# Kernel tuning notes

Measured on AMD Instinct MI355X. Metric: run time of the kernel, lower is better.

The kernel has to match this reference:

```python
import jax, jax.numpy as jnp
import numpy as np
import math

B, S, D_IN, D, H, L, NC = 4, 2048, 64, 512, 8, 2, 2
DK = D // H
FACTOR = 5
TOPK = min(FACTOR * int(math.log(S)), S)  # 35
EPS = 1e-5


def make_pe():
    # sinusoidal positional encoding [S, D]
    pos = jnp.arange(S, dtype=jnp.float32)[:, None]
    div = jnp.exp(jnp.arange(0, D, 2, dtype=jnp.float32) * (-math.log(10000.0) / D))
    pe = jnp.zeros((S, D), jnp.float32)
    pe = pe.at[:, 0::2].set(jnp.sin(pos * div)).at[:, 1::2].set(jnp.cos(pos * div))
    return pe


def layernorm(x, g, b):
    m = x.mean(-1, keepdims=True)
    v = x.var(-1, keepdims=True)
    return (x - m) / jnp.sqrt(v + EPS) * g + b


def setup_inputs() -> dict:
    key = jax.random.key(0)
    ks = iter(jax.random.split(key, 16))
    def p(shape, s=0.02):
        return jax.random.normal(next(ks), shape, jnp.float32) * s
    return dict(
        x=jax.random.normal(next(ks), (B, S, D_IN), jnp.float32),
        emb_w=p((D_IN, D)), emb_b=jnp.zeros((D,), jnp.float32),
        wq=p((L, D, D)), bq=jnp.zeros((L, D), jnp.float32),
        wk=p((L, D, D)), bk=jnp.zeros((L, D), jnp.float32),
        wv=p((L, D, D)), bv=jnp.zeros((L, D), jnp.float32),
        wo=p((L, D, D)), bo=jnp.zeros((L, D), jnp.float32),
        ff1_w=p((L, D, 4 * D)), ff1_b=jnp.zeros((L, 4 * D), jnp.float32),
        ff2_w=p((L, 4 * D, D)), ff2_b=jnp.zeros((L, D), jnp.float32),
        ln1_g=jnp.ones((L, D), jnp.float32), ln1_b=jnp.zeros((L, D), jnp.float32),
        ln2_g=jnp.ones((L, D), jnp.float32), ln2_b=jnp.zeros((L, D), jnp.float32),
        dec1_w=p((D, D // 2)), dec1_b=jnp.zeros((D // 2,), jnp.float32),
        dec2_w=p((D // 2, NC)), dec2_b=jnp.zeros((NC,), jnp.float32),
    )


def reference(x, emb_w, emb_b, wq, bq, wk, bk, wv, bv, wo, bo,
              ff1_w, ff1_b, ff2_w, ff2_b, ln1_g, ln1_b, ln2_g, ln2_b,
              dec1_w, dec1_b, dec2_w, dec2_b):
    h = x @ emb_w + emb_b + make_pe()[None]  # [B,S,D]
    scale = 1.0 / math.sqrt(DK)
    for i in range(L):
        q = (h @ wq[i] + bq[i]).reshape(B, S, H, DK).transpose(0, 2, 1, 3)
        k = (h @ wk[i] + bk[i]).reshape(B, S, H, DK).transpose(0, 2, 1, 3)
        v = (h @ wv[i] + bv[i]).reshape(B, S, H, DK).transpose(0, 2, 1, 3)
        scores = jnp.einsum('bhqd,bhkd->bhqk', q, k) * scale  # [B,H,S,S]
        top_scores, _ = jax.lax.top_k(scores, TOPK)            # [B,H,S,TOPK]
        attn = jax.nn.softmax(top_scores, axis=-1)
        # NOTE: faithful to source quirk — V sliced to its FIRST TOPK rows,
        # top_indices are discarded by the original module.
        ao = jnp.einsum('bhqk,bhkd->bhqd', attn, v[:, :, :TOPK, :])
        ao = ao.transpose(0, 2, 1, 3).reshape(B, S, D) @ wo[i] + bo[i]
        h = layernorm(h + ao, ln1_g[i], ln1_b[i])
        ff = jax.nn.relu(h @ ff1_w[i] + ff1_b[i]) @ ff2_w[i] + ff2_b[i]
        h = layernorm(h + ff, ln2_g[i], ln2_b[i])
    pooled = h.mean(axis=1)  # AdaptiveAvgPool1d(1) over seq
    out = jax.nn.relu(pooled @ dec1_w + dec1_b) @ dec2_w + dec2_b  # [B,NC]
    return out
```

## Files before the change

kernel.cpp:

```cpp
#include <hip/hip_runtime.h>
#include <cmath>

typedef unsigned short u16;
typedef __attribute__((ext_vector_type(8))) short short8;
typedef __attribute__((ext_vector_type(4))) float float4v;
typedef unsigned short ushort2v __attribute__((ext_vector_type(2)));

#define S_LEN 2048
#define NTOK  8192
#define TOPK  35
#define NT512 ((size_t)NTOK*512)

__device__ __forceinline__ u16 f2b(float f){
  unsigned int x = __float_as_uint(f);
  unsigned int r = (x + 0x7fffu + ((x >> 16) & 1u)) >> 16;
  return (u16)r;
}
__device__ __forceinline__ float b2f(u16 u){
  return __uint_as_float(((unsigned int)u) << 16);
}

__device__ __forceinline__ unsigned key_of(float f){
  unsigned u = (unsigned)f2b(f);
  unsigned m = (u & 0x8000u) ? 0xFFFFu : 0x8000u;
  return (u ^ m) & 0xFFFFu;
}
__device__ __forceinline__ float key_to_f(unsigned key){
  unsigned m = (key & 0x8000u) ? 0x8000u : 0xFFFFu;
  return __uint_as_float(((key ^ m) & 0xFFFFu) << 16);
}
__device__ __forceinline__ unsigned pkmax(unsigned a, unsigned b){
  union { unsigned u; ushort2v v; } x, y, r;
  x.u = a; y.u = b;
  r.v = __builtin_elementwise_max(x.v, y.v);
  return r.u;
}
__device__ __forceinline__ unsigned pkmin(unsigned a, unsigned b){
  union { unsigned u; ushort2v v; } x, y, r;
  x.u = a; y.u = b;
  r.v = __builtin_elementwise_min(x.v, y.v);
  return r.u;
}

__device__ __forceinline__ void bsort128(unsigned &v0, unsigned &v1, int l){
  #pragma unroll
  for (int k = 2; k <= 128; k <<= 1){
    #pragma unroll
    for (int j = k >> 1; j > 0; j >>= 1){
      if (j == 64){
        unsigned hi = pkmax(v0, v1), lo = pkmin(v0, v1);
        v0 = hi; v1 = lo;
      } else {
        unsigned o0 = (unsigned)__shfl_xor((int)v0, j, 64);
        unsigned o1 = (unsigned)__shfl_xor((int)v1, j, 64);
        bool up0 = (((l & k) == 0) != ((l & j) != 0));
        bool up1 = ((((64 + l) & k) == 0) != ((l & j) != 0));
        unsigned hi0 = pkmax(v0, o0), lo0 = pkmin(v0, o0);
        unsigned hi1 = pkmax(v1, o1), lo1 = pkmin(v1, o1);
        v0 = up0 ? hi0 : lo0;
        v1 = up1 ? hi1 : lo1;
      }
    }
  }
}

__device__ __forceinline__ void gload16(const void* g, void* l){
  __builtin_amdgcn_global_load_lds(
      (const __attribute__((address_space(1))) unsigned int*)g,
      (__attribute__((address_space(3))) unsigned int*)l, 16, 0, 0);
}

struct WtArgs {
  const float* wq; const float* wk; const float* wv; const float* wo;
  const float* ff1w; const float* ff2w;
  u16* wt_qkv; u16* wt_wo; u16* wt_ff1; u16* wt_ff2;
};
__global__ void prep_kernel(WtArgs a,
                            const float* __restrict__ x, const float* __restrict__ w,
                            const float* __restrict__ bias, float* __restrict__ h,
                            u16* __restrict__ h16){
  __shared__ float xs[4][64];
  __shared__ u16 t[32][33];
  int bx = blockIdx.x;
  int tid = threadIdx.x;
  if (bx < 6144){
    int l  = (bx >= 3072) ? 1 : 0;
    int tt = bx - l*3072;
    const float* W; u16* Wt; int K, N, tx_, ty_;
    if (tt < 1024){
      int seg = tt >> 8, r = tt & 255;
      tx_ = r & 15; ty_ = r >> 4; K = 512; N = 512;
      if (seg == 0){ W = a.wq + (size_t)l*262144; Wt = a.wt_qkv + (size_t)l*786432; }
      else if (seg == 1){ W = a.wk + (size_t)l*262144; Wt = a.wt_qkv + (size_t)l*786432 + 262144; }
      else if (seg == 2){ W = a.wv + (size_t)l*262144; Wt = a.wt_qkv + (size_t)l*786432 + 524288; }
      else { W = a.wo + (size_t)l*262144; Wt = a.wt_wo + (size_t)l*262144; }
    } else if (tt < 2048){
      int r = tt - 1024;
      tx_ = r & 63; ty_ = r >> 6; K = 512; N = 2048;
      W = a.ff1w + (size_t)l*1048576; Wt = a.wt_ff1 + (size_t)l*1048576;
    } else {
      int r = tt - 2048;
      tx_ = r & 15; ty_ = r >> 4; K = 2048; N = 512;
      W = a.ff2w + (size_t)l*1048576; Wt = a.wt_ff2 + (size_t)l*1048576;
    }
    int k0 = ty_*32, n0 = tx_*32;
    int tx = tid & 31, ty = tid >> 5;
    #pragma unroll
    for (int i = ty; i < 32; i += 8)
      t[i][tx] = f2b(W[(size_t)(k0+i)*N + n0+tx]);
    __syncthreads();
    #pragma unroll
    for (int i = ty; i < 32; i += 8)
      Wt[(size_t)(n0+i)*K + k0+tx] = t[tx][i];
  } else {
    int t0 = (bx - 6144) * 4;
    xs[tid >> 6][tid & 63] = x[(size_t)(t0 + (tid >> 6))*64 + (tid & 63)];
    __syncthreads();
    float b0 = bias[tid], b1 = bias[tid + 256];
    float acc[4][2];
    #pragma unroll
    for (int tk = 0; tk < 4; ++tk){ acc[tk][0] = b0; acc[tk][1] = b1; }
    #pragma unroll 8
    for (int k = 0; k < 64; ++k){
      float w0 = w[k*512 + tid];
      float w1 = w[k*512 + tid + 256];
      #pragma unroll
      for (int tk = 0; tk < 4; ++tk){
        float xv = xs[tk][k];
        acc[tk][0] += xv * w0;
        acc[tk][1] += xv * w1;
      }
    }
    const float neg_ln1e4_over_D = -9.210340371976184f / 512.f;
    int c0 = tid, c1 = tid + 256;
    float e0 = expf((float)(c0 & ~1) * neg_ln1e4_over_D);
    float e1 = expf((float)(c1 & ~1) * neg_ln1e4_over_D);
    #pragma unroll
    for (int tk = 0; tk < 4; ++tk){
      int tok = t0 + tk;
      int s = tok & (S_LEN - 1);
      float a0 = (float)s * e0;
      float p0 = (c0 & 1) ? cosf(a0) : sinf(a0);
      float a1 = (float)s * e1;
      float p1 = (c1 & 1) ? cosf(a1) : sinf(a1);
      float v0 = acc[tk][0] + p0, v1 = acc[tk][1] + p1;
      h[(size_t)tok*512 + c0] = v0;  h16[(size_t)tok*512 + c0] = f2b(v0);
      h[(size_t)tok*512 + c1] = v1;  h16[(size_t)tok*512 + c1] = f2b(v1);
    }
  }
}

template<int EPI>
__global__ __launch_bounds__(256) void gemm_mfma(
    const u16* __restrict__ A, int lda, const u16* __restrict__ Bt, int ldb,
    const float* __restrict__ bias0, const float* __restrict__ bias1,
    const float* __restrict__ bias2,
    float* __restrict__ Cf, u16* __restrict__ C16a, u16* __restrict__ C16b,
    float* __restrict__ Cv, int M, int N, int Klen){
  __shared__ __align__(16) u16 As[128*64];
  __shared__ __align__(16) u16 Bs[128*64];
  int tid = threadIdx.x;
  int w = tid >> 6, l = tid & 63, quad = l >> 4, m = l & 15;
  int gx = gridDim.x;
  int orig = blockIdx.y * gx + blockIdx.x;
  int nwg  = gx * gridDim.y;
  int tt   = (orig & 7) * (nwg >> 3) + (orig >> 3);
  int m0 = (tt / gx) * 128, n0 = (tt % gx) * 128;
  int mh = (w >> 1)*64, nh = (w & 1)*64;
  float4v acc[4][4];
  #pragma unroll
  for (int i = 0; i < 4; ++i)
    #pragma unroll
    for (int j = 0; j < 4; ++j) acc[i][j] = (float4v){0.f,0.f,0.f,0.f};

  for (int kt = 0; kt < Klen; kt += 64){
    #pragma unroll
    for (int c = 0; c < 4; ++c){
      int g = c*256 + tid;
      int row = g >> 3, sc = g & 7, dc = sc ^ (row & 7);
      gload16(A  + (size_t)(m0+row)*lda + kt + dc*8, As + (size_t)g*8);
      gload16(Bt + (size_t)(n0+row)*ldb + kt + dc*8, Bs + (size_t)g*8);
    }
    __syncthreads();
    #pragma unroll
    for (int kk = 0; kk < 2; ++kk){
      short8 af[4], bf[4];
      #pragma unroll
      for (int i = 0; i < 4; ++i){
        int dcx = kk*4 + quad;
        int ra = mh + i*16 + m;
        af[i] = *(const short8*)(As + (size_t)(ra*8 + (dcx ^ (ra & 7)))*8);
        int rb = nh + i*16 + m;
        bf[i] = *(const short8*)(Bs + (size_t)(rb*8 + (dcx ^ (rb & 7)))*8);
      }
      #pragma unroll
      for (int i = 0; i < 4; ++i)
        #pragma unroll
        for (int j = 0; j < 4; ++j)
          acc[i][j] = __builtin_amdgcn_mfma_f32_16x16x32_bf16(af[i], bf[j], acc[i][j], 0, 0, 0);
    }
    __syncthreads();
  }

  #pragma unroll
  for (int i = 0; i < 4; ++i){
    #pragma unroll
    for (int j = 0; j < 4; ++j){
      int col = n0 + nh + j*16 + m;
      #pragma unroll
      for (int r = 0; r < 4; ++r){
        int row = m0 + mh + i*16 + quad*4 + r;
        float v = acc[i][j][r];
        if (EPI == 0){
          Cf[(size_t)row*N + col] = v + bias0[col];
        } else if (EPI == 1){
          C16a[(size_t)row*N + col] = f2b(fmaxf(v + bias0[col], 0.f));
        } else {
          int sel = col >> 9, n5 = col & 511;
          const float* bp = (sel == 0) ? bias0 : (sel == 1) ? bias1 : bias2;
          float vv = v + bp[n5];
          int d = n5 & 63, hh = n5 >> 6;
          int b = row >> 11, s = row & 2047;
          size_t idx = (((size_t)(b*8 + hh))*2048 + s)*64 + d;
          if (sel == 0)      C16a[idx] = f2b(vv);
          else if (sel == 1) C16b[idx] = f2b(vv);
          else               Cv[idx]  = vv;
        }
      }
    }
  }
}

__global__ __launch_bounds__(512, 8) void attn_mfma_topk(
    const u16* __restrict__ qb16, const u16* __restrict__ kb16,
    const float* __restrict__ vb, u16* __restrict__ aob16){
  __shared__ unsigned pr[8*1024];
  int tid  = threadIdx.x;
  int w    = tid >> 6, l = tid & 63;
  int quad = l >> 4,  m = l & 15;
  int orig = blockIdx.y * 128 + blockIdx.x;
  int t4   = ((orig & 7) << 9) | (orig >> 3);
  int bh   = t4 >> 7;
  int q0   = (t4 & 127) << 4;

  const u16* Qp = qb16 + ((size_t)bh*2048 + q0 + m)*64 + quad*8;
  short8 a0 = *(const short8*)Qp;
  short8 a1 = *(const short8*)(Qp + 32);

  const u16* Kbase = kb16 + (size_t)bh*2048*64;
  unsigned sc[32];
  int swz = (quad & 1) << 4;
  const u16* kp0 = Kbase + (size_t)(w*128 + m)*64 + quad*8;
  const uint4* p4 = (const uint4*)(pr + w*1024);

  short8 cb0 = *(const short8*)kp0;
  short8 cb1 = *(const short8*)(kp0 + 32);
  #pragma unroll
  for (int t = 0; t < 16; ++t){
    short8 nb0, nb1;
    if (t < 15){
      int tn = t + 1;
      const u16* np = kp0 + (size_t)(((tn >> 3) << 10) + ((tn & 7) << 4))*64;
      nb0 = *(const short8*)np;
      nb1 = *(const short8*)(np + 32);
    }
    float4v acc = {0.f, 0.f, 0.f, 0.f};
    acc = __builtin_amdgcn_mfma_f32_16x16x32_bf16(a0, cb0, acc, 0, 0, 0);
    acc = __builtin_amdgcn_mfma_f32_16x16x32_bf16(a1, cb1, acc, 0, 0, 0);
    int lk = (w << 7) + ((t & 7) << 4);
    #pragma unroll
    for (int c = 0; c < 2; ++c){
      unsigned lo = key_of(acc[2*c]);
      unsigned hi = key_of(acc[2*c+1]);
      pr[(quad*2 + c)*1024 + ((lk + m) ^ swz)] = lo | (hi << 16);
    }
    cb0 = nb0; cb1 = nb1;
    if (t == 7){
      __syncthreads();
      #pragma unroll
      for (int j = 0; j < 4; ++j){
        uint4 v4 = p4[j*64 + l];
        sc[j*4+0] = v4.x; sc[j*4+1] = v4.y; sc[j*4+2] = v4.z; sc[j*4+3] = v4.w;
      }
      __syncthreads();
    }
  }
  __syncthreads();
  #pragma unroll
  for (int j = 0; j < 4; ++j){
    uint4 v4 = p4[j*64 + l];
    sc[16+j*4+0] = v4.x; sc[16+j*4+1] = v4.y; sc[16+j*4+2] = v4.z; sc[16+j*4+3] = v4.w;
  }

  unsigned* row = &pr[w*1024];

  unsigned m1 = pkmax(sc[0], sc[1]);
  unsigned m2 = pkmin(sc[0], sc[1]);
  #pragma unroll
  for (int i = 2; i < 32; ++i){
    unsigned v = sc[i];
    unsigned nm1 = pkmax(m1, v);
    m2 = pkmax(m2, pkmin(m1, v));
    m1 = nm1;
  }

  unsigned mA1 = m1 & 0xFFFFu, mB1 = m1 >> 16;
  unsigned mA2 = m2 & 0xFFFFu, mB2 = m2 >> 16;
  unsigned tA = 0, tB = 0;
  #pragma unroll
  for (int bit = 15; bit >= 0; --bit){
    unsigned cA = tA | (1u << bit);
    unsigned cB = tB | (1u << bit);
    int nA = __popcll(__ballot(mA1 >= cA)) + __popcll(__ballot(mA2 >= cA));
    int nB = __popcll(__ballot(mB1 >= cB)) + __popcll(__ballot(mB2 >= cB));
    if (nA >= TOPK) tA = cA;
    if (nB >= TOPK) tB = cB;
  }
  unsigned TT = (tA - 1) | ((tB - 1) << 16);

  unsigned mask = 0;
  #pragma unroll
  for (int i = 0; i < 32; ++i){
    mask |= (pkmax(sc[i], TT) != TT) ? (1u << i) : 0u;
  }
  int cnt = __popc(mask);

  int pre = cnt;
  #pragma unroll
  for (int off = 1; off < 64; off <<= 1){
    int n = __shfl_up(pre, off, 64);
    if (l >= off) pre += n;
  }
  pre -= cnt;

  #pragma unroll
  for (int i = 0; i < 32; ++i){
    if (mask & (1u << i)){
      int p = pre + __popc(mask & ((1u << i) - 1u));
      if (p < 128) row[p] = sc[i];
    }
  }
  int tot = __shfl(pre + cnt, 63, 64);

  unsigned c0 = (l < tot)      ? row[l]      : 0u;
  unsigned c1 = (64 + l < tot) ? row[64 + l] : 0u;

  const float* Vb = vb + (size_t)bh*2048*64 + l;
  float vreg[TOPK];
  #pragma unroll
  for (int r = 0; r < TOPK; ++r) vreg[r] = Vb[(size_t)r*64];

  bsort128(c0, c1, l);

  unsigned top0 = (unsigned)__shfl((int)c0, 0, 64);
  float mAf = key_to_f(top0 & 0xFFFFu) * 0.125f;
  float mBf = key_to_f(top0 >> 16)     * 0.125f;
  float tvA = key_to_f(c0 & 0xFFFFu)   * 0.125f;
  float tvB = key_to_f(c0 >> 16)       * 0.125f;
  float wAv = (l < TOPK) ? __expf(tvA - mAf) : 0.f;
  float wBv = (l < TOPK) ? __expf(tvB - mBf) : 0.f;

  float dA = wAv, dB = wBv;
  #pragma unroll
  for (int off = 32; off > 0; off >>= 1){
    dA += __shfl_xor(dA, off, 64);
    dB += __shfl_xor(dB, off, 64);
  }

  float accA = 0.f, accB = 0.f;
  #pragma unroll
  for (int r = 0; r < TOPK; ++r){
    float wA = __uint_as_float((unsigned)__builtin_amdgcn_readlane((int)__float_as_uint(wAv), r));
    float wB = __uint_as_float((unsigned)__builtin_amdgcn_readlane((int)__float_as_uint(wBv), r));
    float vv = vreg[r];
    accA += wA * vv;
    accB += wB * vv;
  }
  accA *= __builtin_amdgcn_rcpf(dA);
  accB *= __builtin_amdgcn_rcpf(dB);

  int b = bh >> 3, hh = bh & 7;
  int sA = q0 + w*2;
  aob16[(((size_t)(b*2048 + sA))*8 + hh)*64 + l]     = f2b(accA);
  aob16[(((size_t)(b*2048 + sA + 1))*8 + hh)*64 + l] = f2b(accB);
}

__global__ void resid_ln_kernel(float* __restrict__ h, const float* __restrict__ t,
                                const float* __restrict__ g, const float* __restrict__ b,
                                u16* __restrict__ h16){
  int half = threadIdx.x >> 7;
  int tok  = blockIdx.x*2 + half;
  int tid  = threadIdx.x & 127;
  size_t base4 = (size_t)tok * 128;
  float4 hv = ((const float4*)h)[base4 + tid];
  float4 tv = ((const float4*)t)[base4 + tid];
  float x0 = hv.x + tv.x, x1 = hv.y + tv.y;
  float x2 = hv.z + tv.z, x3 = hv.w + tv.w;
  __shared__ float red[8];
  int wid = threadIdx.x >> 6, lane = threadIdx.x & 63;

  float s = (x0 + x1) + (x2 + x3);
  #pragma unroll
  for (int off = 32; off > 0; off >>= 1) s += __shfl_xor(s, off, 64);
  if (lane == 0) red[wid] = s;
  __syncthreads();
  int hb = half << 1;
  float mean = (red[hb] + red[hb+1]) * (1.f/512.f);

  float d0 = x0 - mean, d1 = x1 - mean, d2 = x2 - mean, d3 = x3 - mean;
  float sq = (d0*d0 + d1*d1) + (d2*d2 + d3*d3);
  #pragma unroll
  for (int off = 32; off > 0; off >>= 1) sq += __shfl_xor(sq, off, 64);
  if (lane == 0) red[4 + wid] = sq;
  __syncthreads();
  float var = (red[4 + hb] + red[4 + hb + 1]) * (1.f/512.f);
  float inv = rsqrtf(var + 1e-5f);
  float4 gv = ((const float4*)g)[tid];
  float4 bv = ((const float4*)b)[tid];
  float o0 = d0 * inv * gv.x + bv.x;
  float o1 = d1 * inv * gv.y + bv.y;
  float o2 = d2 * inv * gv.z + bv.z;
  float o3 = d3 * inv * gv.w + bv.w;
  ((float4*)h)[base4 + tid] = make_float4(o0, o1, o2, o3);
  uint2 pk;
  pk.x = (unsigned)f2b(o0) | ((unsigned)f2b(o1) << 16);
  pk.y = (unsigned)f2b(o2) | ((unsigned)f2b(o3) << 16);
  ((uint2*)h16)[base4 + tid] = pk;
}

__global__ void pool_kernel(const float* __restrict__ h, float* __restrict__ part){
  int c = blockIdx.x * 256 + threadIdx.x;
  int b = blockIdx.y;
  int z = blockIdx.z;
  const float* p = h + ((size_t)b * 2048 + z * 64) * 512 + c;
  float acc = 0.f;
  #pragma unroll 8
  for (int s = 0; s < 64; ++s) acc += p[(size_t)s * 512];
  part[((size_t)(z*4 + b))*512 + c] = acc;
}

__global__ void decoder_kernel(const float* __restrict__ part,
                               const float* __restrict__ w1, const float* __restrict__ b1,
                               const float* __restrict__ w2, const float* __restrict__ b2,
                               float* __restrict__ out){
  __shared__ float ps[4][512];
  __shared__ float hid[4][256];
  int tid = threadIdx.x;
  for (int i = tid; i < 2048; i += 256){
    int b = i >> 9, c = i & 511;
    float s = 0.f;
    #pragma unroll
    for (int z = 0; z < 32; ++z) s += part[((size_t)(z*4 + b))*512 + c];
    ps[b][c] = s * (1.f/2048.f);
  }
  __syncthreads();
  float bb = b1[tid];
  for (int b = 0; b < 4; ++b){
    float acc = bb;
    for (int k = 0; k < 512; ++k) acc += ps[b][k] * w1[k*256 + tid];
    hid[b][tid] = fmaxf(acc, 0.f);
  }
  __syncthreads();
  if (tid < 8){
    int b = tid >> 1, c = tid & 1;
    float acc = b2[c];
    for (int j = 0; j < 256; ++j) acc += hid[b][j] * w2[j*2 + c];
    out[b*2 + c] = acc;
  }
}

extern "C" void kernel_launch(void* const* d_in, const int* in_sizes, int n_in,
                              void* d_out, int out_size, void* d_ws, size_t ws_size,
                              hipStream_t stream){
  const float* x     = (const float*)d_in[0];
  const float* emb_w = (const float*)d_in[1];
  const float* emb_b = (const float*)d_in[2];
  const float* wq    = (const float*)d_in[3];
  const float* bq    = (const float*)d_in[4];
  const float* wk    = (const float*)d_in[5];
  const float* bk    = (const float*)d_in[6];
  const float* wv    = (const float*)d_in[7];
  const float* bv    = (const float*)d_in[8];
  const float* wo    = (const float*)d_in[9];
  const float* bo    = (const float*)d_in[10];
  const float* ff1w  = (const float*)d_in[11];
  const float* ff1b  = (const float*)d_in[12];
  const float* ff2w  = (const float*)d_in[13];
  const float* ff2b  = (const float*)d_in[14];
  const float* ln1g  = (const float*)d_in[15];
  const float* ln1b  = (const float*)d_in[16];
  const float* ln2g  = (const float*)d_in[17];
  const float* ln2b  = (const float*)d_in[18];
  const float* d1w   = (const float*)d_in[19];
  const float* d1b   = (const float*)d_in[20];
  const float* d2w   = (const float*)d_in[21];
  const float* d2b   = (const float*)d_in[22];

  float* h      = (float*)d_ws;
  float* tmp    = h + NT512;
  u16*   u      = (u16*)(tmp + NT512);
  u16*   h16    = u;
  u16*   q16    = u + NT512;
  u16*   k16    = u + 2*NT512;
  float* vb     = (float*)(u + 3*NT512);
  u16*   ff16   = q16;
  u16*   aob16  = (u16*)(vb + NT512);
  u16*   wt     = aob16 + NT512;
  u16*   wt_qkv = wt;
  u16*   wt_wo  = wt_qkv + (size_t)2*1536*512;
  u16*   wt_ff1 = wt_wo  + (size_t)2*512*512;
  u16*   wt_ff2 = wt_ff1 + (size_t)2*2048*512;
  float* part   = tmp;

  WtArgs wa{wq, wk, wv, wo, ff1w, ff2w, wt_qkv, wt_wo, wt_ff1, wt_ff2};
  prep_kernel<<<8192, 256, 0, stream>>>(wa, x, emb_w, emb_b, h, h16);

  for (int l = 0; l < 2; ++l){
    gemm_mfma<2><<<dim3(12, 64), 256, 0, stream>>>(
        h16, 512, wt_qkv + (size_t)l*1536*512, 512,
        bq + l*512, bk + l*512, bv + l*512,
        nullptr, q16, k16, vb, NTOK, 1536, 512);

    attn_mfma_topk<<<dim3(128, 32), 512, 0, stream>>>(q16, k16, vb, aob16);

    gemm_mfma<0><<<dim3(4, 64), 256, 0, stream>>>(
        aob16, 512, wt_wo + (size_t)l*512*512, 512,
        bo + l*512, nullptr, nullptr,
        tmp, nullptr, nullptr, nullptr, NTOK, 512, 512);
    resid_ln_kernel<<<NTOK/2, 256, 0, stream>>>(h, tmp, ln1g + l*512, ln1b + l*512, h16);

    gemm_mfma<1><<<dim3(16, 64), 256, 0, stream>>>(
        h16, 512, wt_ff1 + (size_t)l*2048*512, 512,
        ff1b + l*2048, nullptr, nullptr,
        nullptr, ff16, nullptr, nullptr, NTOK, 2048, 512);

    gemm_mfma<0><<<dim3(4, 64), 256, 0, stream>>>(
        ff16, 2048, wt_ff2 + (size_t)l*512*2048, 2048,
        ff2b + l*512, nullptr, nullptr,
        tmp, nullptr, nullptr, nullptr, NTOK, 512, 2048);
    resid_ln_kernel<<<NTOK/2, 256, 0, stream>>>(h, tmp, ln2g + l*512, ln2b + l*512, h16);
  }

  pool_kernel<<<dim3(2, 4, 32), 256, 0, stream>>>(h, part);
  decoder_kernel<<<1, 256, 0, stream>>>(part, d1w, d1b, d2w, d2b, (float*)d_out);
}
```

Baseline: 709.9 us.

## Double-buffer LDS tiles in MFMA GEMM to overlap loads with compute

```diff
diff --git a/kernel.cpp b/kernel.cpp
--- a/kernel.cpp
+++ b/kernel.cpp
@@ -157,8 +157,8 @@
     const float* __restrict__ bias2,
     float* __restrict__ Cf, u16* __restrict__ C16a, u16* __restrict__ C16b,
     float* __restrict__ Cv, int M, int N, int Klen){
-  __shared__ __align__(16) u16 As[128*64];
-  __shared__ __align__(16) u16 Bs[128*64];
+  __shared__ __align__(16) u16 As[2*128*64];
+  __shared__ __align__(16) u16 Bs[2*128*64];
   int tid = threadIdx.x;
   int w = tid >> 6, l = tid & 63, quad = l >> 4, m = l & 15;
   int gx = gridDim.x;
@@ -173,15 +173,23 @@
     #pragma unroll
     for (int j = 0; j < 4; ++j) acc[i][j] = (float4v){0.f,0.f,0.f,0.f};
 
+  #define GSTAGE(ofs, kt) do { \
+    _Pragma("unroll") \
+    for (int c = 0; c < 4; ++c){ \
+      int g = c*256 + tid; \
+      int row = g >> 3, scx = g & 7, dc = scx ^ (row & 7); \
+      gload16(A  + (size_t)(m0+row)*lda + (kt) + dc*8, As + (ofs) + (size_t)g*8); \
+      gload16(Bt + (size_t)(n0+row)*ldb + (kt) + dc*8, Bs + (ofs) + (size_t)g*8); \
+    } } while(0)
+
+  GSTAGE(0, 0);
+  __syncthreads();
+  int cur = 0;
   for (int kt = 0; kt < Klen; kt += 64){
-    #pragma unroll
-    for (int c = 0; c < 4; ++c){
-      int g = c*256 + tid;
-      int row = g >> 3, sc = g & 7, dc = sc ^ (row & 7);
-      gload16(A  + (size_t)(m0+row)*lda + kt + dc*8, As + (size_t)g*8);
-      gload16(Bt + (size_t)(n0+row)*ldb + kt + dc*8, Bs + (size_t)g*8);
-    }
-    __syncthreads();
+    int nxt = cur ^ 1;
+    if (kt + 64 < Klen) GSTAGE(nxt*(128*64), kt + 64);
+    const u16* Ac = As + cur*(128*64);
+    const u16* Bc = Bs + cur*(128*64);
     #pragma unroll
     for (int kk = 0; kk < 2; ++kk){
       short8 af[4], bf[4];
@@ -189,9 +197,9 @@
       for (int i = 0; i < 4; ++i){
         int dcx = kk*4 + quad;
         int ra = mh + i*16 + m;
-        af[i] = *(const short8*)(As + (size_t)(ra*8 + (dcx ^ (ra & 7)))*8);
+        af[i] = *(const short8*)(Ac + (size_t)(ra*8 + (dcx ^ (ra & 7)))*8);
         int rb = nh + i*16 + m;
-        bf[i] = *(const short8*)(Bs + (size_t)(rb*8 + (dcx ^ (rb & 7)))*8);
+        bf[i] = *(const short8*)(Bc + (size_t)(rb*8 + (dcx ^ (rb & 7)))*8);
       }
       #pragma unroll
       for (int i = 0; i < 4; ++i)
@@ -200,7 +208,9 @@
           acc[i][j] = __builtin_amdgcn_mfma_f32_16x16x32_bf16(af[i], bf[j], acc[i][j], 0, 0, 0);
     }
     __syncthreads();
-  }
+    cur = nxt;
+  }
+  #undef GSTAGE
 
   #pragma unroll
   for (int i = 0; i < 4; ++i){
```

New measurement: 699.5 us. No clear change (-1.5%).
